# Optimization experiments

Hardware: AMD Instinct MI355X
Metric: run time of the kernel (lower is better)

Reference implementation:

```python
import jax, jax.numpy as jnp
import numpy as np

N = 50000       # num_entities / nodes
E = 100000      # edges
K = 8           # incoming edge-graph neighbors per edge
D_NODE = 64
D_EDGE = 64
H = 4
DH = D_EDGE // H
DIN = D_EDGE + 2 * D_NODE  # [edge_feat, node_feat[src], node_feat[dst]]


def setup_inputs() -> dict:
    key = jax.random.key(0)
    ks = jax.random.split(key, 6)
    node_features = jax.random.normal(ks[0], (N, D_NODE), jnp.float32)
    edge_features = jax.random.normal(ks[1], (E, D_EDGE), jnp.float32)
    edge_index = jax.random.randint(ks[2], (2, E), 0, N)
    node_tiers = jax.random.randint(ks[3], (N,), 0, 4, dtype=jnp.int32)
    # edge adjacency (line graph): each edge attends to K other edges
    adj_dst = jnp.repeat(jnp.arange(E), K)                       # [A]
    adj_src = jax.random.randint(ks[4], (E * K,), 0, E)          # [A]
    # learned params: two EdgeAttention layers, each Wq/Wk/Wv [DIN,D_EDGE], Wo [D_EDGE,D_EDGE]
    wkeys = jax.random.split(ks[5], 8)
    def w(k, fan_in, fan_out):
        return jax.random.normal(k, (fan_in, fan_out), jnp.float32) * np.float32(1.0 / np.sqrt(fan_in))
    params = {}
    for li in (1, 2):
        base = (li - 1) * 4
        params[f'l{li}_Wq'] = w(wkeys[base + 0], DIN, D_EDGE)
        params[f'l{li}_Wk'] = w(wkeys[base + 1], DIN, D_EDGE)
        params[f'l{li}_Wv'] = w(wkeys[base + 2], DIN, D_EDGE)
        params[f'l{li}_Wo'] = w(wkeys[base + 3], D_EDGE, D_EDGE)
    return dict(node_features=node_features, edge_features=edge_features,
                edge_index=edge_index, node_tiers=node_tiers,
                adj_src=adj_src, adj_dst=adj_dst, **params)


def _edge_attention(node_f, edge_f, edge_index, adj_src, adj_dst, Wq, Wk, Wv, Wo):
    # x: edge feature conditioned on endpoint node features  [E, DIN]
    x = jnp.concatenate([edge_f, node_f[edge_index[0]], node_f[edge_index[1]]], axis=-1)
    q = (x @ Wq).reshape(E, H, DH)
    k = (x @ Wk).reshape(E, H, DH)
    v = (x @ Wv).reshape(E, H, DH)
    scale = np.float32(1.0 / np.sqrt(DH))
    # scores per adjacency pair  [A, H]
    s = jnp.einsum('ahd,ahd->ah', q[adj_dst], k[adj_src]) * scale
    # segment softmax over incoming neighbors of each dst edge
    m = jax.ops.segment_max(s, adj_dst, num_segments=E)          # [E, H]
    e = jnp.exp(s - m[adj_dst])                                   # [A, H]
    denom = jax.ops.segment_sum(e, adj_dst, num_segments=E)      # [E, H]
    alpha = e / denom[adj_dst]                                    # [A, H]
    out = jax.ops.segment_sum(alpha[..., None] * v[adj_src], adj_dst, num_segments=E)  # [E,H,DH]
    return edge_f + out.reshape(E, D_EDGE) @ Wo                   # residual


def reference(node_features, edge_features, edge_index, node_tiers, adj_src, adj_dst,
              l1_Wq, l1_Wk, l1_Wv, l1_Wo, l2_Wq, l2_Wk, l2_Wv, l2_Wo):
    ef = _edge_attention(node_features, edge_features, edge_index, adj_src, adj_dst,
                         l1_Wq, l1_Wk, l1_Wv, l1_Wo)
    ef = _edge_attention(node_features, ef, edge_index, adj_src, adj_dst,
                         l2_Wq, l2_Wk, l2_Wv, l2_Wo)
    return ef  # updated edge features of the output DeltaGraph
```

## Files before the change

kernel.cpp:

```cpp
#include <hip/hip_runtime.h>

#define NE 100000
#define NN 50000

typedef short short8 __attribute__((ext_vector_type(8)));
typedef float f32x4 __attribute__((ext_vector_type(4)));
typedef unsigned short ushort;
typedef unsigned int uint;

__device__ inline ushort f2bf(float f) {
    unsigned int u = __float_as_uint(f);
    u += 0x7FFFu + ((u >> 16) & 1u);
    return (ushort)(u >> 16);
}
__device__ inline float bf2f(ushort u) {
    return __uint_as_float((unsigned int)u << 16);
}

__device__ inline short8 pack_bf8(float4 a, float4 b) {
    short8 r;
    r[0] = (short)f2bf(a.x); r[1] = (short)f2bf(a.y);
    r[2] = (short)f2bf(a.z); r[3] = (short)f2bf(a.w);
    r[4] = (short)f2bf(b.x); r[5] = (short)f2bf(b.y);
    r[6] = (short)f2bf(b.z); r[7] = (short)f2bf(b.w);
    return r;
}

__device__ inline void pack_qkv_slot(int slot, const float* Wq, const float* Wk,
                                     const float* Wv, ushort* wf)
{
    int lane = slot & 63;
    int st = slot >> 6;
    int s = st / 12, t = st % 12;
    int n = t * 16 + (lane & 15);
    int kb = s * 32 + (lane >> 4) * 8;
    const float* w = (n < 64) ? Wq : (n < 128) ? Wk : Wv;
    int nn = n & 63;
    #pragma unroll
    for (int j = 0; j < 8; ++j)
        wf[(size_t)slot * 8 + j] = f2bf(w[(size_t)(kb + j) * 64 + nn]);
}

__device__ inline void pack_wo_slot(int slot, const float* Wo, ushort* wf)
{
    int lane = slot & 63;
    int st = slot >> 6;
    int s = st / 4, t = st % 4;
    int n = t * 16 + (lane & 15);
    int kb = s * 32 + (lane >> 4) * 8;
    #pragma unroll
    for (int j = 0; j < 8; ++j)
        wf[(size_t)slot * 8 + j] = f2bf(Wo[(size_t)(kb + j) * 64 + n]);
}

__global__ __launch_bounds__(256) void prep_all(
    const float* __restrict__ l1Wq, const float* __restrict__ l1Wk,
    const float* __restrict__ l1Wv, const float* __restrict__ l1Wo,
    const float* __restrict__ l2Wq, const float* __restrict__ l2Wk,
    const float* __restrict__ l2Wv, const float* __restrict__ l2Wo,
    ushort* __restrict__ wf1, ushort* __restrict__ wf2,
    ushort* __restrict__ wo1, ushort* __restrict__ wo2)
{
    int idx = blockIdx.x * 256 + threadIdx.x;
    if (idx < 4608)            pack_qkv_slot(idx,         l1Wq, l1Wk, l1Wv, wf1);
    else if (idx < 9216)       pack_qkv_slot(idx - 4608,  l2Wq, l2Wk, l2Wv, wf2);
    else if (idx < 9728)       pack_wo_slot (idx - 9216,  l1Wo, wo1);
    else if (idx < 10240)      pack_wo_slot (idx - 9728,  l2Wo, wo2);
}

#define MFMA_B16(a, b, c) c = __builtin_amdgcn_mfma_f32_16x16x32_bf16(a, b, c, 0, 0, 0)

#define GLP const __attribute__((address_space(1))) uint*
#define LDP __attribute__((address_space(3))) uint*

#define STAGE(ph) do {                                                         \
    const char* gs_ = (const char*)wfrag + (size_t)(ph) * 24576 + (size_t)l * 16; \
    __builtin_amdgcn_global_load_lds((GLP)(gs_ + (size_t)(w*6+0)*1024), (LDP)(ldsb + (size_t)(w*6+0)*1024), 16, 0, 0); \
    __builtin_amdgcn_global_load_lds((GLP)(gs_ + (size_t)(w*6+1)*1024), (LDP)(ldsb + (size_t)(w*6+1)*1024), 16, 0, 0); \
    __builtin_amdgcn_global_load_lds((GLP)(gs_ + (size_t)(w*6+2)*1024), (LDP)(ldsb + (size_t)(w*6+2)*1024), 16, 0, 0); \
    __builtin_amdgcn_global_load_lds((GLP)(gs_ + (size_t)(w*6+3)*1024), (LDP)(ldsb + (size_t)(w*6+3)*1024), 16, 0, 0); \
    __builtin_amdgcn_global_load_lds((GLP)(gs_ + (size_t)(w*6+4)*1024), (LDP)(ldsb + (size_t)(w*6+4)*1024), 16, 0, 0); \
    __builtin_amdgcn_global_load_lds((GLP)(gs_ + (size_t)(w*6+5)*1024), (LDP)(ldsb + (size_t)(w*6+5)*1024), 16, 0, 0); \
} while (0)

#define KSTEP(Areg, si) do {                                                   \
    const char* lb_ = ldsb + (size_t)(si) * 12288 + (size_t)l * 16;            \
    short8 b0_  = *(const short8*)(lb_ + 0);                                   \
    short8 b1_  = *(const short8*)(lb_ + 1024);                                \
    short8 b2_  = *(const short8*)(lb_ + 2048);                                \
    short8 b3_  = *(const short8*)(lb_ + 3072);                                \
    short8 b4_  = *(const short8*)(lb_ + 4096);                                \
    short8 b5_  = *(const short8*)(lb_ + 5120);                                \
    short8 b6_  = *(const short8*)(lb_ + 6144);                                \
    short8 b7_  = *(const short8*)(lb_ + 7168);                                \
    short8 b8_  = *(const short8*)(lb_ + 8192);                                \
    short8 b9_  = *(const short8*)(lb_ + 9216);                                \
    short8 b10_ = *(const short8*)(lb_ + 10240);                               \
    short8 b11_ = *(const short8*)(lb_ + 11264);                               \
    MFMA_B16(Areg, b0_,  c0);  MFMA_B16(Areg, b1_,  c1);                       \
    MFMA_B16(Areg, b2_,  c2);  MFMA_B16(Areg, b3_,  c3);                       \
    MFMA_B16(Areg, b4_,  c4);  MFMA_B16(Areg, b5_,  c5);                       \
    MFMA_B16(Areg, b6_,  c6);  MFMA_B16(Areg, b7_,  c7);                       \
    MFMA_B16(Areg, b8_,  c8);  MFMA_B16(Areg, b9_,  c9);                       \
    MFMA_B16(Areg, b10_, c10); MFMA_B16(Areg, b11_, c11);                      \
} while (0)

#define STORE_T(creg, dstp, cloc) do {                                         \
    ushort* dp_ = (dstp) + (cloc);                                             \
    int row_ = e0 + kg * 4;                                                    \
    if (row_ + 0 < NE) dp_[(size_t)(row_ + 0) * 64] = f2bf(creg[0]);           \
    if (row_ + 1 < NE) dp_[(size_t)(row_ + 1) * 64] = f2bf(creg[1]);           \
    if (row_ + 2 < NE) dp_[(size_t)(row_ + 2) * 64] = f2bf(creg[2]);           \
    if (row_ + 3 < NE) dp_[(size_t)(row_ + 3) * 64] = f2bf(creg[3]);           \
} while (0)

__global__ __launch_bounds__(256) void qkv_mfma(
    const float* __restrict__ ef, const float* __restrict__ nodef,
    const int* __restrict__ eidx, const ushort* __restrict__ wfrag,
    ushort* __restrict__ qo, ushort* __restrict__ ko, ushort* __restrict__ vo)
{
    __shared__ __align__(1024) char ldsb[24 * 1024];

    const int tid = threadIdx.x;
    const int l   = tid & 63;
    const int w   = tid >> 6;
    const int r   = l & 15;
    const int kg  = l >> 4;
    const int e0  = blockIdx.x * 64 + w * 16;
    const int e   = e0 + r;
    const int ec  = (e < NE) ? e : NE - 1;

    STAGE(0);

    const int koff = kg * 8;
    const float* rp0 = ef    + (size_t)ec * 64;
    const float* rp1 = nodef + (size_t)eidx[ec] * 64;
    const float* rp2 = nodef + (size_t)eidx[NE + ec] * 64;

    short8 A0 = pack_bf8(*(const float4*)(rp0 + koff),      *(const float4*)(rp0 + koff + 4));
    short8 A1 = pack_bf8(*(const float4*)(rp0 + 32 + koff), *(const float4*)(rp0 + 36 + koff));
    short8 A2 = pack_bf8(*(const float4*)(rp1 + koff),      *(const float4*)(rp1 + koff + 4));
    short8 A3 = pack_bf8(*(const float4*)(rp1 + 32 + koff), *(const float4*)(rp1 + 36 + koff));
    short8 A4 = pack_bf8(*(const float4*)(rp2 + koff),      *(const float4*)(rp2 + koff + 4));
    short8 A5 = pack_bf8(*(const float4*)(rp2 + 32 + koff), *(const float4*)(rp2 + 36 + koff));

    f32x4 c0 = (f32x4)(0.f), c1 = (f32x4)(0.f), c2  = (f32x4)(0.f), c3  = (f32x4)(0.f);
    f32x4 c4 = (f32x4)(0.f), c5 = (f32x4)(0.f), c6  = (f32x4)(0.f), c7  = (f32x4)(0.f);
    f32x4 c8 = (f32x4)(0.f), c9 = (f32x4)(0.f), c10 = (f32x4)(0.f), c11 = (f32x4)(0.f);

    __syncthreads();
    KSTEP(A0, 0);
    KSTEP(A1, 1);
    __syncthreads();
    STAGE(1);
    __syncthreads();
    KSTEP(A2, 0);
    KSTEP(A3, 1);
    __syncthreads();
    STAGE(2);
    __syncthreads();
    KSTEP(A4, 0);
    KSTEP(A5, 1);

    STORE_T(c0,  qo, 0 * 16 + r);
    STORE_T(c1,  qo, 1 * 16 + r);
    STORE_T(c2,  qo, 2 * 16 + r);
    STORE_T(c3,  qo, 3 * 16 + r);
    STORE_T(c4,  ko, 0 * 16 + r);
    STORE_T(c5,  ko, 1 * 16 + r);
    STORE_T(c6,  ko, 2 * 16 + r);
    STORE_T(c7,  ko, 3 * 16 + r);
    STORE_T(c8,  vo, 0 * 16 + r);
    STORE_T(c9,  vo, 1 * 16 + r);
    STORE_T(c10, vo, 2 * 16 + r);
    STORE_T(c11, vo, 3 * 16 + r);
}

__global__ __launch_bounds__(256) void attn_kernel(
    const ushort* __restrict__ q, const ushort* __restrict__ kbuf,
    const ushort* __restrict__ vbuf, const int* __restrict__ adj_src,
    ushort* __restrict__ ao)
{
    const int wid  = (blockIdx.x * 256 + threadIdx.x) >> 6;
    const int lane = threadIdx.x & 63;
    if (wid >= NE) return;
    const int e    = wid;
    const int half = lane >> 5;
    const int l32  = lane & 31;

    const int4 nb = *(const int4*)(adj_src + e * 8 + half * 4);
    const int nbr0 = nb.x, nbr1 = nb.y, nbr2 = nb.z, nbr3 = nb.w;

    ushort2 qu = *(const ushort2*)(q + (size_t)e * 64 + l32 * 2);
    const float q0 = bf2f(qu.x), q1 = bf2f(qu.y);

    ushort2 ku0 = *(const ushort2*)(kbuf + (size_t)nbr0 * 64 + l32 * 2);
    ushort2 ku1 = *(const ushort2*)(kbuf + (size_t)nbr1 * 64 + l32 * 2);
    ushort2 ku2 = *(const ushort2*)(kbuf + (size_t)nbr2 * 64 + l32 * 2);
    ushort2 ku3 = *(const ushort2*)(kbuf + (size_t)nbr3 * 64 + l32 * 2);
    ushort2 vu0 = *(const ushort2*)(vbuf + (size_t)nbr0 * 64 + l32 * 2);
    ushort2 vu1 = *(const ushort2*)(vbuf + (size_t)nbr1 * 64 + l32 * 2);
    ushort2 vu2 = *(const ushort2*)(vbuf + (size_t)nbr2 * 64 + l32 * 2);
    ushort2 vu3 = *(const ushort2*)(vbuf + (size_t)nbr3 * 64 + l32 * 2);

    float s0 = q0 * bf2f(ku0.x) + q1 * bf2f(ku0.y);
    float s1 = q0 * bf2f(ku1.x) + q1 * bf2f(ku1.y);
    float s2 = q0 * bf2f(ku2.x) + q1 * bf2f(ku2.y);
    float s3 = q0 * bf2f(ku3.x) + q1 * bf2f(ku3.y);
    s0 += __shfl_xor(s0, 1); s0 += __shfl_xor(s0, 2); s0 += __shfl_xor(s0, 4);
    s1 += __shfl_xor(s1, 1); s1 += __shfl_xor(s1, 2); s1 += __shfl_xor(s1, 4);
    s2 += __shfl_xor(s2, 1); s2 += __shfl_xor(s2, 2); s2 += __shfl_xor(s2, 4);
    s3 += __shfl_xor(s3, 1); s3 += __shfl_xor(s3, 2); s3 += __shfl_xor(s3, 4);
    s0 *= 0.25f; s1 *= 0.25f; s2 *= 0.25f; s3 *= 0.25f;

    float m = fmaxf(fmaxf(s0, s1), fmaxf(s2, s3));
    m = fmaxf(m, __shfl_xor(m, 32));
    float w0 = __expf(s0 - m), w1 = __expf(s1 - m);
    float w2 = __expf(s2 - m), w3 = __expf(s3 - m);
    float den = w0 + w1 + w2 + w3;
    den += __shfl_xor(den, 32);
    const float inv = 1.f / den;

    float ox = 0.f, oy = 0.f;
    ox = fmaf(w0, bf2f(vu0.x), ox); oy = fmaf(w0, bf2f(vu0.y), oy);
    ox = fmaf(w1, bf2f(vu1.x), ox); oy = fmaf(w1, bf2f(vu1.y), oy);
    ox = fmaf(w2, bf2f(vu2.x), ox); oy = fmaf(w2, bf2f(vu2.y), oy);
    ox = fmaf(w3, bf2f(vu3.x), ox); oy = fmaf(w3, bf2f(vu3.y), oy);
    ox = (ox + __shfl_xor(ox, 32)) * inv;
    oy = (oy + __shfl_xor(oy, 32)) * inv;

    if (lane < 32) {
        ushort2 o;
        o.x = f2bf(ox);
        o.y = f2bf(oy);
        *(ushort2*)(ao + (size_t)e * 64 + l32 * 2) = o;
    }
}

__global__ __launch_bounds__(256) void wo_mfma(
    const float* __restrict__ ef_in, const ushort* __restrict__ attn,
    const ushort* __restrict__ wofrag, float* __restrict__ efo)
{
    const int wave = threadIdx.x >> 6;
    const int lane = threadIdx.x & 63;
    const int r  = lane & 15;
    const int kg = lane >> 4;
    const int e0 = blockIdx.x * 64 + wave * 16;
    const int e  = e0 + r;
    const int ec = (e < NE) ? e : NE - 1;

    short8 af0 = *(const short8*)(attn + (size_t)ec * 64 + kg * 8);
    short8 af1 = *(const short8*)(attn + (size_t)ec * 64 + 32 + kg * 8);

    const char* wf = (const char*)wofrag + (size_t)lane * 16;
    f32x4 d0 = (f32x4)(0.f), d1 = (f32x4)(0.f), d2 = (f32x4)(0.f), d3 = (f32x4)(0.f);
    short8 g0 = *(const short8*)(wf + 0 * 1024);
    short8 g1 = *(const short8*)(wf + 1 * 1024);
    short8 g2 = *(const short8*)(wf + 2 * 1024);
    short8 g3 = *(const short8*)(wf + 3 * 1024);
    MFMA_B16(af0, g0, d0); MFMA_B16(af0, g1, d1);
    MFMA_B16(af0, g2, d2); MFMA_B16(af0, g3, d3);
    g0 = *(const short8*)(wf + 4 * 1024);
    g1 = *(const short8*)(wf + 5 * 1024);
    g2 = *(const short8*)(wf + 6 * 1024);
    g3 = *(const short8*)(wf + 7 * 1024);
    MFMA_B16(af1, g0, d0); MFMA_B16(af1, g1, d1);
    MFMA_B16(af1, g2, d2); MFMA_B16(af1, g3, d3);

    const int orow = e0 + kg * 4;
    #pragma unroll
    for (int t = 0; t < 4; ++t) {
        const f32x4 dd = (t == 0) ? d0 : (t == 1) ? d1 : (t == 2) ? d2 : d3;
        const int c = t * 16 + r;
        #pragma unroll
        for (int j = 0; j < 4; ++j) {
            int row = orow + j;
            if (row < NE) {
                size_t off = (size_t)row * 64 + c;
                efo[off] = dd[j] + ef_in[off];
            }
        }
    }
}

extern "C" void kernel_launch(void* const* d_in, const int* in_sizes, int n_in,
                              void* d_out, int out_size, void* d_ws, size_t ws_size,
                              hipStream_t stream)
{
    const float* nodef   = (const float*)d_in[0];
    const float* ef      = (const float*)d_in[1];
    const int*   eidx    = (const int*)d_in[2];
    const int*   adj_src = (const int*)d_in[4];
    const float* l1Wq = (const float*)d_in[6];
    const float* l1Wk = (const float*)d_in[7];
    const float* l1Wv = (const float*)d_in[8];
    const float* l1Wo = (const float*)d_in[9];
    const float* l2Wq = (const float*)d_in[10];
    const float* l2Wk = (const float*)d_in[11];
    const float* l2Wv = (const float*)d_in[12];
    const float* l2Wo = (const float*)d_in[13];

    ushort* q  = (ushort*)d_ws;
    ushort* k  = q  + (size_t)NE * 64;
    ushort* v  = k  + (size_t)NE * 64;
    ushort* ao = v  + (size_t)NE * 64;
    ushort* wf1 = ao + (size_t)NE * 64;
    ushort* wf2 = wf1 + 36864;
    ushort* wo1 = wf2 + 36864;
    ushort* wo2 = wo1 + 4096;
    float* out = (float*)d_out;

    dim3 blk(256);
    const int gq = (NE + 63) / 64;
    const int ga = (NE + 3) / 4;
    const int gw = (NE + 63) / 64;

    prep_all<<<40, blk, 0, stream>>>(l1Wq, l1Wk, l1Wv, l1Wo,
                                     l2Wq, l2Wk, l2Wv, l2Wo,
                                     wf1, wf2, wo1, wo2);

    qkv_mfma<<<gq, blk, 0, stream>>>(ef, nodef, eidx, wf1, q, k, v);
    attn_kernel<<<ga, blk, 0, stream>>>(q, k, v, adj_src, ao);
    wo_mfma<<<gw, blk, 0, stream>>>(ef, ao, wo1, out);
    qkv_mfma<<<gq, blk, 0, stream>>>(out, nodef, eidx, wf2, q, k, v);
    attn_kernel<<<ga, blk, 0, stream>>>(q, k, v, adj_src, ao);
    wo_mfma<<<gw, blk, 0, stream>>>(out, ao, wo2, out);
}
```

Baseline: 149.2 us.

## Stage QKV outputs through LDS for coalesced stores; add direct-weight variant for layer two

The QKV projection kernel now writes its MFMA accumulators into a padded LDS tile and then stores full 16-byte rows to global memory, instead of scattered 2-byte stores. A second variant for layer two processes 32 edges per block, with each wave owning three output column tiles. It reads weight fragments directly from global memory instead of staging them into LDS with global_load_lds. The aim is to cut uncoalesced write traffic and the barrier and staging overhead. The cost is duplicated kernels and heavier register use in the new variant.

```diff
diff --git a/kernel.cpp b/kernel.cpp
--- a/kernel.cpp
+++ b/kernel.cpp
@@ -69,7 +69,6 @@
 }
 
 #define MFMA_B16(a, b, c) c = __builtin_amdgcn_mfma_f32_16x16x32_bf16(a, b, c, 0, 0, 0)
-
 #define GLP const __attribute__((address_space(1))) uint*
 #define LDP __attribute__((address_space(3))) uint*
 
@@ -105,21 +104,18 @@
     MFMA_B16(Areg, b10_, c10); MFMA_B16(Areg, b11_, c11);                      \
 } while (0)
 
-#define STORE_T(creg, dstp, cloc) do {                                         \
-    ushort* dp_ = (dstp) + (cloc);                                             \
-    int row_ = e0 + kg * 4;                                                    \
-    if (row_ + 0 < NE) dp_[(size_t)(row_ + 0) * 64] = f2bf(creg[0]);           \
-    if (row_ + 1 < NE) dp_[(size_t)(row_ + 1) * 64] = f2bf(creg[1]);           \
-    if (row_ + 2 < NE) dp_[(size_t)(row_ + 2) * 64] = f2bf(creg[2]);           \
-    if (row_ + 3 < NE) dp_[(size_t)(row_ + 3) * 64] = f2bf(creg[3]);           \
+#define DUMPA(creg, t_lit) do {                                                \
+    ushort* p_ = lds_u + wbu + (kg * 4) * 200 + (t_lit) * 16 + r;              \
+    p_[0]   = f2bf(creg[0]); p_[200] = f2bf(creg[1]);                          \
+    p_[400] = f2bf(creg[2]); p_[600] = f2bf(creg[3]);                          \
 } while (0)
 
-__global__ __launch_bounds__(256) void qkv_mfma(
+__global__ __launch_bounds__(256) void qkv_mfma_a(
     const float* __restrict__ ef, const float* __restrict__ nodef,
     const int* __restrict__ eidx, const ushort* __restrict__ wfrag,
     ushort* __restrict__ qo, ushort* __restrict__ ko, ushort* __restrict__ vo)
 {
-    __shared__ __align__(1024) char ldsb[24 * 1024];
+    __shared__ __align__(1024) char ldsb[25600];
 
     const int tid = threadIdx.x;
     const int l   = tid & 63;
@@ -161,19 +157,113 @@
     __syncthreads();
     KSTEP(A4, 0);
     KSTEP(A5, 1);
-
-    STORE_T(c0,  qo, 0 * 16 + r);
-    STORE_T(c1,  qo, 1 * 16 + r);
-    STORE_T(c2,  qo, 2 * 16 + r);
-    STORE_T(c3,  qo, 3 * 16 + r);
-    STORE_T(c4,  ko, 0 * 16 + r);
-    STORE_T(c5,  ko, 1 * 16 + r);
-    STORE_T(c6,  ko, 2 * 16 + r);
-    STORE_T(c7,  ko, 3 * 16 + r);
-    STORE_T(c8,  vo, 0 * 16 + r);
-    STORE_T(c9,  vo, 1 * 16 + r);
-    STORE_T(c10, vo, 2 * 16 + r);
-    STORE_T(c11, vo, 3 * 16 + r);
+    __syncthreads();
+
+    ushort* lds_u = (ushort*)ldsb;
+    const int wbu = w * 3200;
+    DUMPA(c0, 0);  DUMPA(c1, 1);  DUMPA(c2, 2);  DUMPA(c3, 3);
+    DUMPA(c4, 4);  DUMPA(c5, 5);  DUMPA(c6, 6);  DUMPA(c7, 7);
+    DUMPA(c8, 8);  DUMPA(c9, 9);  DUMPA(c10, 10); DUMPA(c11, 11);
+    __builtin_amdgcn_s_waitcnt(0);
+
+    const int row16 = l >> 2;
+    const int seg   = l & 3;
+    const int grow  = e0 + row16;
+    if (grow < NE) {
+        const ushort* rp = lds_u + wbu + row16 * 200;
+        ushort* dq = qo + (size_t)grow * 64 + seg * 16;
+        ushort* dk = ko + (size_t)grow * 64 + seg * 16;
+        ushort* dv = vo + (size_t)grow * 64 + seg * 16;
+        *(short8*)(dq + 0) = *(const short8*)(rp +   0 + seg * 16 + 0);
+        *(short8*)(dq + 8) = *(const short8*)(rp +   0 + seg * 16 + 8);
+        *(short8*)(dk + 0) = *(const short8*)(rp +  64 + seg * 16 + 0);
+        *(short8*)(dk + 8) = *(const short8*)(rp +  64 + seg * 16 + 8);
+        *(short8*)(dv + 0) = *(const short8*)(rp + 128 + seg * 16 + 0);
+        *(short8*)(dv + 8) = *(const short8*)(rp + 128 + seg * 16 + 8);
+    }
+}
+
+#define BSTEP(s_lit, A0reg, A1reg) do {                                        \
+    const char* bp_ = (const char*)wfrag + (size_t)((s_lit) * 12 + 3 * w) * 1024 \
+                      + (size_t)l * 16;                                        \
+    short8 bb0_ = *(const short8*)(bp_ + 0);                                   \
+    short8 bb1_ = *(const short8*)(bp_ + 1024);                                \
+    short8 bb2_ = *(const short8*)(bp_ + 2048);                                \
+    MFMA_B16(A0reg, bb0_, d00); MFMA_B16(A0reg, bb1_, d01);                    \
+    MFMA_B16(A0reg, bb2_, d02);                                                \
+    MFMA_B16(A1reg, bb0_, d10); MFMA_B16(A1reg, bb1_, d11);                    \
+    MFMA_B16(A1reg, bb2_, d12);                                                \
+} while (0)
+
+#define DUMPB(dreg, T_lit, n_lit) do {                                         \
+    ushort* p_ = ldso + ((T_lit) * 16 + kg * 4) * 200 + (3 * w + (n_lit)) * 16 + r; \
+    p_[0]   = f2bf(dreg[0]); p_[200] = f2bf(dreg[1]);                          \
+    p_[400] = f2bf(dreg[2]); p_[600] = f2bf(dreg[3]);                          \
+} while (0)
+
+__global__ __launch_bounds__(256) void qkv_mfma_b(
+    const float* __restrict__ ef, const float* __restrict__ nodef,
+    const int* __restrict__ eidx, const ushort* __restrict__ wfrag,
+    ushort* __restrict__ qo, ushort* __restrict__ ko, ushort* __restrict__ vo)
+{
+    __shared__ __align__(16) ushort ldso[32 * 200];
+
+    const int tid = threadIdx.x;
+    const int l   = tid & 63;
+    const int w   = tid >> 6;
+    const int r   = l & 15;
+    const int kg  = l >> 4;
+    const int e0  = blockIdx.x * 32;
+
+    const int ea  = e0 + r;
+    const int eb  = e0 + 16 + r;
+    const int eac = (ea < NE) ? ea : NE - 1;
+    const int ebc = (eb < NE) ? eb : NE - 1;
+
+    const int koff = kg * 8;
+    const float* a0p = ef    + (size_t)eac * 64;
+    const float* a1p = nodef + (size_t)eidx[eac] * 64;
+    const float* a2p = nodef + (size_t)eidx[NE + eac] * 64;
+    const float* b0p = ef    + (size_t)ebc * 64;
+    const float* b1p = nodef + (size_t)eidx[ebc] * 64;
+    const float* b2p = nodef + (size_t)eidx[NE + ebc] * 64;
+
+    short8 A00 = pack_bf8(*(const float4*)(a0p + koff),      *(const float4*)(a0p + koff + 4));
+    short8 A01 = pack_bf8(*(const float4*)(a0p + 32 + koff), *(const float4*)(a0p + 36 + koff));
+    short8 A02 = pack_bf8(*(const float4*)(a1p + koff),      *(const float4*)(a1p + koff + 4));
+    short8 A03 = pack_bf8(*(const float4*)(a1p + 32 + koff), *(const float4*)(a1p + 36 + koff));
+    short8 A04 = pack_bf8(*(const float4*)(a2p + koff),      *(const float4*)(a2p + koff + 4));
+    short8 A05 = pack_bf8(*(const float4*)(a2p + 32 + koff), *(const float4*)(a2p + 36 + koff));
+    short8 A10 = pack_bf8(*(const float4*)(b0p + koff),      *(const float4*)(b0p + koff + 4));
+    short8 A11 = pack_bf8(*(const float4*)(b0p + 32 + koff), *(const float4*)(b0p + 36 + koff));
+    short8 A12 = pack_bf8(*(const float4*)(b1p + koff),      *(const float4*)(b1p + koff + 4));
+    short8 A13 = pack_bf8(*(const float4*)(b1p + 32 + koff), *(const float4*)(b1p + 36 + koff));
+    short8 A14 = pack_bf8(*(const float4*)(b2p + koff),      *(const float4*)(b2p + koff + 4));
+    short8 A15 = pack_bf8(*(const float4*)(b2p + 32 + koff), *(const float4*)(b2p + 36 + koff));
+
+    f32x4 d00 = (f32x4)(0.f), d01 = (f32x4)(0.f), d02 = (f32x4)(0.f);
+    f32x4 d10 = (f32x4)(0.f), d11 = (f32x4)(0.f), d12 = (f32x4)(0.f);
+
+    BSTEP(0, A00, A10);
+    BSTEP(1, A01, A11);
+    BSTEP(2, A02, A12);
+    BSTEP(3, A03, A13);
+    BSTEP(4, A04, A14);
+    BSTEP(5, A05, A15);
+
+    DUMPB(d00, 0, 0); DUMPB(d01, 0, 1); DUMPB(d02, 0, 2);
+    DUMPB(d10, 1, 0); DUMPB(d11, 1, 1); DUMPB(d12, 1, 2);
+    __syncthreads();
+
+    const int row  = tid >> 3;
+    const int seg  = tid & 7;
+    const int grow = e0 + row;
+    if (grow < NE) {
+        const ushort* rp = ldso + row * 200;
+        *(short8*)(qo + (size_t)grow * 64 + seg * 8) = *(const short8*)(rp +   0 + seg * 8);
+        *(short8*)(ko + (size_t)grow * 64 + seg * 8) = *(const short8*)(rp +  64 + seg * 8);
+        *(short8*)(vo + (size_t)grow * 64 + seg * 8) = *(const short8*)(rp + 128 + seg * 8);
+    }
 }
 
 __global__ __launch_bounds__(256) void attn_kernel(
@@ -311,18 +401,19 @@
     float* out = (float*)d_out;
 
     dim3 blk(256);
-    const int gq = (NE + 63) / 64;
-    const int ga = (NE + 3) / 4;
-    const int gw = (NE + 63) / 64;
+    const int gqa = (NE + 63) / 64;
+    const int gqb = (NE + 31) / 32;
+    const int ga  = (NE + 3) / 4;
+    const int gw  = (NE + 63) / 64;
 
     prep_all<<<40, blk, 0, stream>>>(l1Wq, l1Wk, l1Wv, l1Wo,
                                      l2Wq, l2Wk, l2Wv, l2Wo,
                                      wf1, wf2, wo1, wo2);
 
-    qkv_mfma<<<gq, blk, 0, stream>>>(ef, nodef, eidx, wf1, q, k, v);
+    qkv_mfma_a<<<gqa, blk, 0, stream>>>(ef, nodef, eidx, wf1, q, k, v);
     attn_kernel<<<ga, blk, 0, stream>>>(q, k, v, adj_src, ao);
     wo_mfma<<<gw, blk, 0, stream>>>(ef, ao, wo1, out);
-    qkv_mfma<<<gq, blk, 0, stream>>>(out, nodef, eidx, wf2, q, k, v);
+    qkv_mfma_b<<<gqb, blk, 0, stream>>>(out, nodef, eidx, wf2, q, k, v);
     attn_kernel<<<ga, blk, 0, stream>>>(q, k, v, adj_src, ao);
     wo_mfma<<<gw, blk, 0, stream>>>(out, ao, wo2, out);
 }
```

Result: slower. 165.0 us (+10.6%).

## Precompute per-node Q/K/V projections and stage edge QKV stores through LDS

Applied to the files above, without the earlier changes.

The QKV projection is split by linearity. The node-feature parts of Wq/Wk/Wv are applied once per node into SRC and DST tables of width 192, and each edge then gathers and adds its two rows to a 64-wide edge-feature MFMA. This cuts the per-edge matmul depth from 192 to 64. Output tiles now go through LDS so stores are coalesced 16-byte writes instead of strided 2-byte writes, and the attention output reuses the q buffer. The trade-off is wider bf16 gathers per edge, extra node-table writes for each layer, and an extra bf16 rounding of the partial sums.

```diff
diff --git a/kernel.cpp b/kernel.cpp
--- a/kernel.cpp
+++ b/kernel.cpp
@@ -26,14 +26,22 @@
     return r;
 }
 
-__device__ inline void pack_qkv_slot(int slot, const float* Wq, const float* Wk,
-                                     const float* Wv, ushort* wf)
+__device__ inline short8 add3_bf(short8 a, short8 b, short8 c) {
+    short8 o;
+    #pragma unroll
+    for (int i = 0; i < 8; ++i)
+        o[i] = (short)f2bf(bf2f((ushort)a[i]) + bf2f((ushort)b[i]) + bf2f((ushort)c[i]));
+    return o;
+}
+
+__device__ inline void pack192(int slot, const float* Wq, const float* Wk,
+                               const float* Wv, int row_off, ushort* wf)
 {
     int lane = slot & 63;
     int st = slot >> 6;
     int s = st / 12, t = st % 12;
     int n = t * 16 + (lane & 15);
-    int kb = s * 32 + (lane >> 4) * 8;
+    int kb = row_off + s * 32 + (lane >> 4) * 8;
     const float* w = (n < 64) ? Wq : (n < 128) ? Wk : Wv;
     int nn = n & 63;
     #pragma unroll
@@ -58,29 +66,35 @@
     const float* __restrict__ l1Wv, const float* __restrict__ l1Wo,
     const float* __restrict__ l2Wq, const float* __restrict__ l2Wk,
     const float* __restrict__ l2Wv, const float* __restrict__ l2Wo,
-    ushort* __restrict__ wf1, ushort* __restrict__ wf2,
+    ushort* __restrict__ we1, ushort* __restrict__ we2,
+    ushort* __restrict__ wn1s, ushort* __restrict__ wn1d,
+    ushort* __restrict__ wn2s, ushort* __restrict__ wn2d,
     ushort* __restrict__ wo1, ushort* __restrict__ wo2)
 {
     int idx = blockIdx.x * 256 + threadIdx.x;
-    if (idx < 4608)            pack_qkv_slot(idx,         l1Wq, l1Wk, l1Wv, wf1);
-    else if (idx < 9216)       pack_qkv_slot(idx - 4608,  l2Wq, l2Wk, l2Wv, wf2);
-    else if (idx < 9728)       pack_wo_slot (idx - 9216,  l1Wo, wo1);
-    else if (idx < 10240)      pack_wo_slot (idx - 9728,  l2Wo, wo2);
+    if      (idx < 1536)  pack192(idx,         l1Wq, l1Wk, l1Wv,   0, we1);
+    else if (idx < 3072)  pack192(idx - 1536,  l2Wq, l2Wk, l2Wv,   0, we2);
+    else if (idx < 4608)  pack192(idx - 3072,  l1Wq, l1Wk, l1Wv,  64, wn1s);
+    else if (idx < 6144)  pack192(idx - 4608,  l1Wq, l1Wk, l1Wv, 128, wn1d);
+    else if (idx < 7680)  pack192(idx - 6144,  l2Wq, l2Wk, l2Wv,  64, wn2s);
+    else if (idx < 9216)  pack192(idx - 7680,  l2Wq, l2Wk, l2Wv, 128, wn2d);
+    else if (idx < 9728)  pack_wo_slot(idx - 9216, l1Wo, wo1);
+    else if (idx < 10240) pack_wo_slot(idx - 9728, l2Wo, wo2);
 }
 
 #define MFMA_B16(a, b, c) c = __builtin_amdgcn_mfma_f32_16x16x32_bf16(a, b, c, 0, 0, 0)
-
 #define GLP const __attribute__((address_space(1))) uint*
 #define LDP __attribute__((address_space(3))) uint*
 
-#define STAGE(ph) do {                                                         \
-    const char* gs_ = (const char*)wfrag + (size_t)(ph) * 24576 + (size_t)l * 16; \
-    __builtin_amdgcn_global_load_lds((GLP)(gs_ + (size_t)(w*6+0)*1024), (LDP)(ldsb + (size_t)(w*6+0)*1024), 16, 0, 0); \
-    __builtin_amdgcn_global_load_lds((GLP)(gs_ + (size_t)(w*6+1)*1024), (LDP)(ldsb + (size_t)(w*6+1)*1024), 16, 0, 0); \
-    __builtin_amdgcn_global_load_lds((GLP)(gs_ + (size_t)(w*6+2)*1024), (LDP)(ldsb + (size_t)(w*6+2)*1024), 16, 0, 0); \
-    __builtin_amdgcn_global_load_lds((GLP)(gs_ + (size_t)(w*6+3)*1024), (LDP)(ldsb + (size_t)(w*6+3)*1024), 16, 0, 0); \
-    __builtin_amdgcn_global_load_lds((GLP)(gs_ + (size_t)(w*6+4)*1024), (LDP)(ldsb + (size_t)(w*6+4)*1024), 16, 0, 0); \
-    __builtin_amdgcn_global_load_lds((GLP)(gs_ + (size_t)(w*6+5)*1024), (LDP)(ldsb + (size_t)(w*6+5)*1024), 16, 0, 0); \
+#define STAGE24(buf) do {                                                      \
+    const char* gs_ = (const char*)(buf) + (size_t)l * 16;                     \
+    _Pragma("unroll")                                                          \
+    for (int i_ = 0; i_ < 6; ++i_) {                                           \
+        const int fr_ = w * 6 + i_;                                            \
+        __builtin_amdgcn_global_load_lds((GLP)(gs_ + (size_t)fr_ * 1024),      \
+                                         (LDP)(ldsb + (size_t)fr_ * 1024),    \
+                                         16, 0, 0);                            \
+    }                                                                          \
 } while (0)
 
 #define KSTEP(Areg, si) do {                                                   \
@@ -105,44 +119,36 @@
     MFMA_B16(Areg, b10_, c10); MFMA_B16(Areg, b11_, c11);                      \
 } while (0)
 
-#define STORE_T(creg, dstp, cloc) do {                                         \
-    ushort* dp_ = (dstp) + (cloc);                                             \
-    int row_ = e0 + kg * 4;                                                    \
-    if (row_ + 0 < NE) dp_[(size_t)(row_ + 0) * 64] = f2bf(creg[0]);           \
-    if (row_ + 1 < NE) dp_[(size_t)(row_ + 1) * 64] = f2bf(creg[1]);           \
-    if (row_ + 2 < NE) dp_[(size_t)(row_ + 2) * 64] = f2bf(creg[2]);           \
-    if (row_ + 3 < NE) dp_[(size_t)(row_ + 3) * 64] = f2bf(creg[3]);           \
+#define DUMPA(creg, t_lit) do {                                                \
+    ushort* p_ = lds_u + wbu + (kg * 4) * 200 + (t_lit) * 16 + r;              \
+    p_[0]   = f2bf(creg[0]); p_[200] = f2bf(creg[1]);                          \
+    p_[400] = f2bf(creg[2]); p_[600] = f2bf(creg[3]);                          \
 } while (0)
 
-__global__ __launch_bounds__(256) void qkv_mfma(
-    const float* __restrict__ ef, const float* __restrict__ nodef,
-    const int* __restrict__ eidx, const ushort* __restrict__ wfrag,
-    ushort* __restrict__ qo, ushort* __restrict__ ko, ushort* __restrict__ vo)
-{
-    __shared__ __align__(1024) char ldsb[24 * 1024];
+__global__ __launch_bounds__(256) void node_proj(
+    const float* __restrict__ nodef,
+    const ushort* __restrict__ wsrc, const ushort* __restrict__ wdst,
+    ushort* __restrict__ SRC, ushort* __restrict__ DST)
+{
+    __shared__ __align__(1024) char ldsb[25600];
+    const ushort* wfrag = blockIdx.y ? wdst : wsrc;
+    ushort*       TBL   = blockIdx.y ? DST  : SRC;
 
     const int tid = threadIdx.x;
     const int l   = tid & 63;
     const int w   = tid >> 6;
     const int r   = l & 15;
     const int kg  = l >> 4;
-    const int e0  = blockIdx.x * 64 + w * 16;
-    const int e   = e0 + r;
-    const int ec  = (e < NE) ? e : NE - 1;
-
-    STAGE(0);
-
+    const int n0w = blockIdx.x * 64 + w * 16;
+
+    STAGE24(wfrag);
+
+    const int nr  = n0w + r;
+    const int nrc = (nr < NN) ? nr : NN - 1;
+    const float* rp = nodef + (size_t)nrc * 64;
     const int koff = kg * 8;
-    const float* rp0 = ef    + (size_t)ec * 64;
-    const float* rp1 = nodef + (size_t)eidx[ec] * 64;
-    const float* rp2 = nodef + (size_t)eidx[NE + ec] * 64;
-
-    short8 A0 = pack_bf8(*(const float4*)(rp0 + koff),      *(const float4*)(rp0 + koff + 4));
-    short8 A1 = pack_bf8(*(const float4*)(rp0 + 32 + koff), *(const float4*)(rp0 + 36 + koff));
-    short8 A2 = pack_bf8(*(const float4*)(rp1 + koff),      *(const float4*)(rp1 + koff + 4));
-    short8 A3 = pack_bf8(*(const float4*)(rp1 + 32 + koff), *(const float4*)(rp1 + 36 + koff));
-    short8 A4 = pack_bf8(*(const float4*)(rp2 + koff),      *(const float4*)(rp2 + koff + 4));
-    short8 A5 = pack_bf8(*(const float4*)(rp2 + 32 + koff), *(const float4*)(rp2 + 36 + koff));
+    short8 A0 = pack_bf8(*(const float4*)(rp + koff),      *(const float4*)(rp + koff + 4));
+    short8 A1 = pack_bf8(*(const float4*)(rp + 32 + koff), *(const float4*)(rp + 36 + koff));
 
     f32x4 c0 = (f32x4)(0.f), c1 = (f32x4)(0.f), c2  = (f32x4)(0.f), c3  = (f32x4)(0.f);
     f32x4 c4 = (f32x4)(0.f), c5 = (f32x4)(0.f), c6  = (f32x4)(0.f), c7  = (f32x4)(0.f);
@@ -152,28 +158,96 @@
     KSTEP(A0, 0);
     KSTEP(A1, 1);
     __syncthreads();
-    STAGE(1);
+
+    ushort* lds_u = (ushort*)ldsb;
+    const int wbu = w * 3200;
+    DUMPA(c0, 0);  DUMPA(c1, 1);  DUMPA(c2, 2);  DUMPA(c3, 3);
+    DUMPA(c4, 4);  DUMPA(c5, 5);  DUMPA(c6, 6);  DUMPA(c7, 7);
+    DUMPA(c8, 8);  DUMPA(c9, 9);  DUMPA(c10, 10); DUMPA(c11, 11);
+    __builtin_amdgcn_s_waitcnt(0);
+
+    const int row16 = l >> 2;
+    const int seg   = l & 3;
+    const int ng    = n0w + row16;
+    if (ng < NN) {
+        const ushort* lp = lds_u + wbu + row16 * 200 + seg * 16;
+        ushort* op = TBL + (size_t)ng * 192 + seg * 16;
+        *(short8*)(op +   0) = *(const short8*)(lp +   0);
+        *(short8*)(op +   8) = *(const short8*)(lp +   8);
+        *(short8*)(op +  64) = *(const short8*)(lp +  64);
+        *(short8*)(op +  72) = *(const short8*)(lp +  72);
+        *(short8*)(op + 128) = *(const short8*)(lp + 128);
+        *(short8*)(op + 136) = *(const short8*)(lp + 136);
+    }
+}
+
+__global__ __launch_bounds__(256) void edge_qkv(
+    const float* __restrict__ efin, const int* __restrict__ eidx,
+    const ushort* __restrict__ SRC, const ushort* __restrict__ DST,
+    const ushort* __restrict__ wfrag,
+    ushort* __restrict__ qo, ushort* __restrict__ ko, ushort* __restrict__ vo)
+{
+    __shared__ __align__(1024) char ldsb[25600];
+
+    const int tid = threadIdx.x;
+    const int l   = tid & 63;
+    const int w   = tid >> 6;
+    const int r   = l & 15;
+    const int kg  = l >> 4;
+    const int e0w = blockIdx.x * 64 + w * 16;
+
+    STAGE24(wfrag);
+
+    const int row16 = l >> 2;
+    const int seg   = l & 3;
+    const int eg    = e0w + row16;
+    const int egc   = (eg < NE) ? eg : NE - 1;
+    const int srcn  = eidx[egc];
+    const int dstn  = eidx[NE + egc];
+    const ushort* sp = SRC + (size_t)srcn * 192 + seg * 16;
+    const ushort* dp = DST + (size_t)dstn * 192 + seg * 16;
+    short8 gq0 = *(const short8*)(sp +   0), gq1 = *(const short8*)(sp +   8);
+    short8 gk0 = *(const short8*)(sp +  64), gk1 = *(const short8*)(sp +  72);
+    short8 gv0 = *(const short8*)(sp + 128), gv1 = *(const short8*)(sp + 136);
+    short8 hq0 = *(const short8*)(dp +   0), hq1 = *(const short8*)(dp +   8);
+    short8 hk0 = *(const short8*)(dp +  64), hk1 = *(const short8*)(dp +  72);
+    short8 hv0 = *(const short8*)(dp + 128), hv1 = *(const short8*)(dp + 136);
+
+    const int e  = e0w + r;
+    const int ec = (e < NE) ? e : NE - 1;
+    const float* rp = efin + (size_t)ec * 64;
+    const int koff = kg * 8;
+    short8 A0 = pack_bf8(*(const float4*)(rp + koff),      *(const float4*)(rp + koff + 4));
+    short8 A1 = pack_bf8(*(const float4*)(rp + 32 + koff), *(const float4*)(rp + 36 + koff));
+
+    f32x4 c0 = (f32x4)(0.f), c1 = (f32x4)(0.f), c2  = (f32x4)(0.f), c3  = (f32x4)(0.f);
+    f32x4 c4 = (f32x4)(0.f), c5 = (f32x4)(0.f), c6  = (f32x4)(0.f), c7  = (f32x4)(0.f);
+    f32x4 c8 = (f32x4)(0.f), c9 = (f32x4)(0.f), c10 = (f32x4)(0.f), c11 = (f32x4)(0.f);
+
     __syncthreads();
-    KSTEP(A2, 0);
-    KSTEP(A3, 1);
+    KSTEP(A0, 0);
+    KSTEP(A1, 1);
     __syncthreads();
-    STAGE(2);
-    __syncthreads();
-    KSTEP(A4, 0);
-    KSTEP(A5, 1);
-
-    STORE_T(c0,  qo, 0 * 16 + r);
-    STORE_T(c1,  qo, 1 * 16 + r);
-    STORE_T(c2,  qo, 2 * 16 + r);
-    STORE_T(c3,  qo, 3 * 16 + r);
-    STORE_T(c4,  ko, 0 * 16 + r);
-    STORE_T(c5,  ko, 1 * 16 + r);
-    STORE_T(c6,  ko, 2 * 16 + r);
-    STORE_T(c7,  ko, 3 * 16 + r);
-    STORE_T(c8,  vo, 0 * 16 + r);
-    STORE_T(c9,  vo, 1 * 16 + r);
-    STORE_T(c10, vo, 2 * 16 + r);
-    STORE_T(c11, vo, 3 * 16 + r);
+
+    ushort* lds_u = (ushort*)ldsb;
+    const int wbu = w * 3200;
+    DUMPA(c0, 0);  DUMPA(c1, 1);  DUMPA(c2, 2);  DUMPA(c3, 3);
+    DUMPA(c4, 4);  DUMPA(c5, 5);  DUMPA(c6, 6);  DUMPA(c7, 7);
+    DUMPA(c8, 8);  DUMPA(c9, 9);  DUMPA(c10, 10); DUMPA(c11, 11);
+    __builtin_amdgcn_s_waitcnt(0);
+
+    if (eg < NE) {
+        const ushort* lp = lds_u + wbu + row16 * 200 + seg * 16;
+        ushort* oq = qo + (size_t)eg * 64 + seg * 16;
+        ushort* ok = ko + (size_t)eg * 64 + seg * 16;
+        ushort* ov = vo + (size_t)eg * 64 + seg * 16;
+        *(short8*)(oq + 0) = add3_bf(*(const short8*)(lp +   0), gq0, hq0);
+        *(short8*)(oq + 8) = add3_bf(*(const short8*)(lp +   8), gq1, hq1);
+        *(short8*)(ok + 0) = add3_bf(*(const short8*)(lp +  64), gk0, hk0);
+        *(short8*)(ok + 8) = add3_bf(*(const short8*)(lp +  72), gk1, hk1);
+        *(short8*)(ov + 0) = add3_bf(*(const short8*)(lp + 128), gv0, hv0);
+        *(short8*)(ov + 8) = add3_bf(*(const short8*)(lp + 136), gv1, hv1);
+    }
 }
 
 __global__ __launch_bounds__(256) void attn_kernel(
@@ -300,29 +374,37 @@
     const float* l2Wv = (const float*)d_in[12];
     const float* l2Wo = (const float*)d_in[13];
 
-    ushort* q  = (ushort*)d_ws;
-    ushort* k  = q  + (size_t)NE * 64;
-    ushort* v  = k  + (size_t)NE * 64;
-    ushort* ao = v  + (size_t)NE * 64;
-    ushort* wf1 = ao + (size_t)NE * 64;
-    ushort* wf2 = wf1 + 36864;
-    ushort* wo1 = wf2 + 36864;
-    ushort* wo2 = wo1 + 4096;
+    ushort* q   = (ushort*)d_ws;
+    ushort* k   = q   + (size_t)NE * 64;
+    ushort* v   = k   + (size_t)NE * 64;
+    ushort* SRC = v   + (size_t)NE * 64;
+    ushort* DST = SRC + (size_t)NN * 192;
+    ushort* we1  = DST + (size_t)NN * 192;
+    ushort* we2  = we1 + 12288;
+    ushort* wn1s = we2 + 12288;
+    ushort* wn1d = wn1s + 12288;
+    ushort* wn2s = wn1d + 12288;
+    ushort* wn2d = wn2s + 12288;
+    ushort* wo1  = wn2d + 12288;
+    ushort* wo2  = wo1 + 4096;
     float* out = (float*)d_out;
 
     dim3 blk(256);
-    const int gq = (NE + 63) / 64;
+    const int ge = (NE + 63) / 64;
+    const dim3 gn((NN + 63) / 64, 2);
     const int ga = (NE + 3) / 4;
     const int gw = (NE + 63) / 64;
 
     prep_all<<<40, blk, 0, stream>>>(l1Wq, l1Wk, l1Wv, l1Wo,
                                      l2Wq, l2Wk, l2Wv, l2Wo,
-                                     wf1, wf2, wo1, wo2);
-
-    qkv_mfma<<<gq, blk, 0, stream>>>(ef, nodef, eidx, wf1, q, k, v);
-    attn_kernel<<<ga, blk, 0, stream>>>(q, k, v, adj_src, ao);
-    wo_mfma<<<gw, blk, 0, stream>>>(ef, ao, wo1, out);
-    qkv_mfma<<<gq, blk, 0, stream>>>(out, nodef, eidx, wf2, q, k, v);
-    attn_kernel<<<ga, blk, 0, stream>>>(q, k, v, adj_src, ao);
-    wo_mfma<<<gw, blk, 0, stream>>>(out, ao, wo2, out);
-}
+                                     we1, we2, wn1s, wn1d, wn2s, wn2d, wo1, wo2);
+
+    node_proj<<<gn, blk, 0, stream>>>(nodef, wn1s, wn1d, SRC, DST);
+    edge_qkv<<<ge, blk, 0, stream>>>(ef, eidx, SRC, DST, we1, q, k, v);
+    attn_kernel<<<ga, blk, 0, stream>>>(q, k, v, adj_src, q);
+    wo_mfma<<<gw, blk, 0, stream>>>(ef, q, wo1, out);
+    node_proj<<<gn, blk, 0, stream>>>(nodef, wn2s, wn2d, SRC, DST);
+    edge_qkv<<<ge, blk, 0, stream>>>(out, eidx, SRC, DST, we2, q, k, v);
+    attn_kernel<<<ga, blk, 0, stream>>>(q, k, v, adj_src, q);
+    wo_mfma<<<gw, blk, 0, stream>>>(out, q, wo2, out);
+}
```

Result: slower. 175.8 us (+17.8%).

## Split edge/node gather into a separate pre-packing kernel for QKV MFMA

Applied to the files above, without the earlier changes.

Adds a gather_pack kernel that gathers the edge features and both endpoint node features, converts them to bf16 and writes them in the MFMA A-fragment tile layout. qkv_mfma then loads its A operands as fully coalesced short8 reads instead of doing the indexed gathers and fp32-to-bf16 packing itself. The aim is to take the irregular gather latency out of the MFMA kernel. In exchange each layer gets an extra kernel launch and a roughly 38 MB bf16 intermediate that must be written and read back. The last partial block also reads tiles past the end of that buffer, although its stores are guarded.

```diff
diff --git a/kernel.cpp b/kernel.cpp
--- a/kernel.cpp
+++ b/kernel.cpp
@@ -68,8 +68,43 @@
     else if (idx < 10240)      pack_wo_slot (idx - 9728,  l2Wo, wo2);
 }
 
+__global__ __launch_bounds__(256) void gather_pack(
+    const float* __restrict__ efin, const float* __restrict__ nodef,
+    const int* __restrict__ eidx, ushort* __restrict__ xp)
+{
+    const int t = blockIdx.x * 256 + threadIdx.x;
+    const int e = t >> 2;
+    const int p = t & 3;
+    if (e >= NE) return;
+
+    const int src = eidx[e];
+    const int dst = eidx[NE + e];
+    const float* s0 = efin  + (size_t)e   * 64 + p * 16;
+    const float* s1 = nodef + (size_t)src * 64 + p * 16;
+    const float* s2 = nodef + (size_t)dst * 64 + p * 16;
+
+    const int tile = e >> 4;
+    const int r    = e & 15;
+    const int sh   = p >> 1;
+    const int kgA  = (p & 1) * 2;
+
+    #pragma unroll
+    for (int c = 0; c < 3; ++c) {
+        const float* sp = (c == 0) ? s0 : (c == 1) ? s1 : s2;
+        float4 f0 = *(const float4*)(sp + 0);
+        float4 f1 = *(const float4*)(sp + 4);
+        float4 f2 = *(const float4*)(sp + 8);
+        float4 f3 = *(const float4*)(sp + 12);
+        short8 loA = pack_bf8(f0, f1);
+        short8 loB = pack_bf8(f2, f3);
+        const int s = 2 * c + sh;
+        ushort* base = xp + ((size_t)(tile * 6 + s) * 64 + r) * 8;
+        *(short8*)(base + (size_t)(kgA    ) * 16 * 8) = loA;
+        *(short8*)(base + (size_t)(kgA + 1) * 16 * 8) = loB;
+    }
+}
+
 #define MFMA_B16(a, b, c) c = __builtin_amdgcn_mfma_f32_16x16x32_bf16(a, b, c, 0, 0, 0)
-
 #define GLP const __attribute__((address_space(1))) uint*
 #define LDP __attribute__((address_space(3))) uint*
 
@@ -115,8 +150,7 @@
 } while (0)
 
 __global__ __launch_bounds__(256) void qkv_mfma(
-    const float* __restrict__ ef, const float* __restrict__ nodef,
-    const int* __restrict__ eidx, const ushort* __restrict__ wfrag,
+    const ushort* __restrict__ xp, const ushort* __restrict__ wfrag,
     ushort* __restrict__ qo, ushort* __restrict__ ko, ushort* __restrict__ vo)
 {
     __shared__ __align__(1024) char ldsb[24 * 1024];
@@ -127,22 +161,17 @@
     const int r   = l & 15;
     const int kg  = l >> 4;
     const int e0  = blockIdx.x * 64 + w * 16;
-    const int e   = e0 + r;
-    const int ec  = (e < NE) ? e : NE - 1;
+    const int tile = blockIdx.x * 4 + w;
 
     STAGE(0);
 
-    const int koff = kg * 8;
-    const float* rp0 = ef    + (size_t)ec * 64;
-    const float* rp1 = nodef + (size_t)eidx[ec] * 64;
-    const float* rp2 = nodef + (size_t)eidx[NE + ec] * 64;
-
-    short8 A0 = pack_bf8(*(const float4*)(rp0 + koff),      *(const float4*)(rp0 + koff + 4));
-    short8 A1 = pack_bf8(*(const float4*)(rp0 + 32 + koff), *(const float4*)(rp0 + 36 + koff));
-    short8 A2 = pack_bf8(*(const float4*)(rp1 + koff),      *(const float4*)(rp1 + koff + 4));
-    short8 A3 = pack_bf8(*(const float4*)(rp1 + 32 + koff), *(const float4*)(rp1 + 36 + koff));
-    short8 A4 = pack_bf8(*(const float4*)(rp2 + koff),      *(const float4*)(rp2 + koff + 4));
-    short8 A5 = pack_bf8(*(const float4*)(rp2 + 32 + koff), *(const float4*)(rp2 + 36 + koff));
+    const short8* ap = (const short8*)xp + (size_t)tile * 6 * 64 + l;
+    short8 A0 = ap[0 * 64];
+    short8 A1 = ap[1 * 64];
+    short8 A2 = ap[2 * 64];
+    short8 A3 = ap[3 * 64];
+    short8 A4 = ap[4 * 64];
+    short8 A5 = ap[5 * 64];
 
     f32x4 c0 = (f32x4)(0.f), c1 = (f32x4)(0.f), c2  = (f32x4)(0.f), c3  = (f32x4)(0.f);
     f32x4 c4 = (f32x4)(0.f), c5 = (f32x4)(0.f), c6  = (f32x4)(0.f), c7  = (f32x4)(0.f);
@@ -300,17 +329,19 @@
     const float* l2Wv = (const float*)d_in[12];
     const float* l2Wo = (const float*)d_in[13];
 
-    ushort* q  = (ushort*)d_ws;
-    ushort* k  = q  + (size_t)NE * 64;
-    ushort* v  = k  + (size_t)NE * 64;
-    ushort* ao = v  + (size_t)NE * 64;
-    ushort* wf1 = ao + (size_t)NE * 64;
+    ushort* q   = (ushort*)d_ws;
+    ushort* k   = q   + (size_t)NE * 64;
+    ushort* v   = k   + (size_t)NE * 64;
+    ushort* ao  = v   + (size_t)NE * 64;
+    ushort* xp  = ao  + (size_t)NE * 64;
+    ushort* wf1 = xp  + (size_t)NE * 192;
     ushort* wf2 = wf1 + 36864;
     ushort* wo1 = wf2 + 36864;
     ushort* wo2 = wo1 + 4096;
     float* out = (float*)d_out;
 
     dim3 blk(256);
+    const int gp = (NE * 4 + 255) / 256;
     const int gq = (NE + 63) / 64;
     const int ga = (NE + 3) / 4;
     const int gw = (NE + 63) / 64;
@@ -319,10 +350,12 @@
                                      l2Wq, l2Wk, l2Wv, l2Wo,
                                      wf1, wf2, wo1, wo2);
 
-    qkv_mfma<<<gq, blk, 0, stream>>>(ef, nodef, eidx, wf1, q, k, v);
+    gather_pack<<<gp, blk, 0, stream>>>(ef, nodef, eidx, xp);
+    qkv_mfma<<<gq, blk, 0, stream>>>(xp, wf1, q, k, v);
     attn_kernel<<<ga, blk, 0, stream>>>(q, k, v, adj_src, ao);
     wo_mfma<<<gw, blk, 0, stream>>>(ef, ao, wo1, out);
-    qkv_mfma<<<gq, blk, 0, stream>>>(out, nodef, eidx, wf2, q, k, v);
+    gather_pack<<<gp, blk, 0, stream>>>(out, nodef, eidx, xp);
+    qkv_mfma<<<gq, blk, 0, stream>>>(xp, wf2, q, k, v);
     attn_kernel<<<ga, blk, 0, stream>>>(q, k, v, adj_src, ao);
     wo_mfma<<<gw, blk, 0, stream>>>(out, ao, wo2, out);
 }
```

New measurement: 172.7 us. 15.7% more time.
